# Performance work log

Hardware: AMD Instinct MI355X
Metric: run time of the kernel (lower is better)

The kernel has to match this reference:

```python
import jax, jax.numpy as jnp
import numpy as np

B, C, H, W = 8, 512, 96, 96
C8 = C // 8


def conv1x1(x, w, b):
    # x: (B,Cin,H,W), w: (Cout,Cin), b: (Cout,)
    return jnp.einsum('bchw,oc->bohw', x, w) + b[None, :, None, None]


def setup_inputs() -> dict:
    key = jax.random.key(0)
    ks = jax.random.split(key, 12)
    s = 0.05
    return {
        'x_exmplar': jax.random.normal(ks[0], (B, C, H, W), jnp.float32),
        'x_query': jax.random.normal(ks[1], (B, C, H, W), jnp.float32),
        'Wq': jax.random.normal(ks[2], (C8, C), jnp.float32) * s,
        'bq': jax.random.normal(ks[3], (C8,), jnp.float32) * s,
        'Wk': jax.random.normal(ks[4], (C8, C), jnp.float32) * s,
        'bk': jax.random.normal(ks[5], (C8,), jnp.float32) * s,
        'Wv': jax.random.normal(ks[6], (C, C), jnp.float32) * s,
        'bv': jax.random.normal(ks[7], (C,), jnp.float32) * s,
        'Wqv': jax.random.normal(ks[8], (C, C), jnp.float32) * s,
        'bqv': jax.random.normal(ks[9], (C,), jnp.float32) * s,
        'gamma1': jax.random.normal(ks[10], (1,), jnp.float32) * 0.5,
        'gamma2': jax.random.normal(ks[11], (1,), jnp.float32) * 0.5,
    }


def reference(x_exmplar, x_query, Wq, bq, Wk, bk, Wv, bv, Wqv, bqv, gamma1, gamma2):
    Bq, Cq, Hh, Ww = x_query.shape
    q = conv1x1(x_query, Wq, bq)        # (B,C8,H,W)
    k = conv1x1(x_exmplar, Wk, bk)      # (B,C8,H,W)
    v = conv1x1(x_exmplar, Wv, bv)      # (B,C,H,W)
    qv = conv1x1(x_query, Wqv, bqv)     # (B,C,H,W)

    # Criss-cross energies. energy_H masks the self position (INF diag).
    eH = jnp.einsum('bchw,bcjw->bhwj', q, k)            # (B,H,W,H)
    eye = jnp.eye(Hh, dtype=bool)                        # (H,H)
    eH = jnp.where(eye[:, None, :], -jnp.inf, eH)        # mask h==j
    eW = jnp.einsum('bchw,bchj->bhwj', q, k)             # (B,H,W,W)

    att = jax.nn.softmax(jnp.concatenate([eH, eW], axis=3), axis=3)
    att_H, att_W = att[..., :Hh], att[..., Hh:]          # (B,H,W,H),(B,H,W,W)

    out_H = jnp.einsum('bcjw,bhwj->bchw', v, att_H)
    out_W = jnp.einsum('bchj,bhwj->bchw', v, att_W)
    qout_H = jnp.einsum('bcjw,bhwj->bchw', qv, att_H)
    qout_W = jnp.einsum('bchj,bhwj->bchw', qv, att_W)

    # Diagonal (LR/RL) terms. Note: torch.diagonal of the transposed map equals
    # the diagonal itself, so energy_RL == energy_LR (faithful to original).
    qd = jnp.diagonal(q, axis1=2, axis2=3)               # (B,C8,D)
    kd = jnp.diagonal(k, axis1=2, axis2=3)
    vd = jnp.diagonal(v, axis1=2, axis2=3)               # (B,C,D)
    qvd = jnp.diagonal(qv, axis1=2, axis2=3)
    e_LR = jnp.einsum('bci,bcj->bij', kd, qd)            # (B,D,D)

    # softmax over a size-1 trailing axis (as in the original): yields ones,
    # broadcast-added over the width dim.
    out_LR = jax.nn.softmax(jnp.einsum('bcd,bdj->bcj', vd, e_LR)[..., None], axis=3)
    out_RL = jax.nn.softmax(jnp.einsum('bcd,bdj->bcj', vd, e_LR)[..., None], axis=3)
    qout_LR = jax.nn.softmax(jnp.einsum('bcd,bdj->bcj', qvd, e_LR)[..., None], axis=3)
    qout_RL = jax.nn.softmax(jnp.einsum('bcd,bdj->bcj', qvd, e_LR)[..., None], axis=3)

    examplar_att = out_H + out_W + out_LR + out_RL       # (B,C,H,W) via broadcast
    query_att = qout_H + qout_W + qout_LR + qout_RL
    return (gamma1 * examplar_att + x_exmplar, gamma2 * query_att + x_query)
```

## Files before the change

### kernel.cpp

```cpp
#include <hip/hip_runtime.h>
#include <math.h>

#define C_   512
#define C8_  64
#define HH   96
#define WW   96
#define PP   9216
#define CP   4718592
#define C8P  589824
#define ATTN 1769472

typedef __attribute__((ext_vector_type(4))) float f32x4;
typedef __attribute__((ext_vector_type(8))) __bf16 bf16x8;
typedef __attribute__((ext_vector_type(8))) unsigned short ushort8;
typedef __attribute__((ext_vector_type(4))) unsigned short ushort4v;
typedef __attribute__((ext_vector_type(2))) unsigned short ushort2v;
typedef __attribute__((ext_vector_type(2))) float float2v;

__device__ __forceinline__ float bf2f(unsigned short u) {
    union { unsigned u; float f; } x; x.u = ((unsigned)u) << 16; return x.f;
}
__device__ __forceinline__ unsigned short f2bf(float f) {
    union { float f; unsigned u; } x; x.f = f;
    unsigned r = x.u + 0x7fffu + ((x.u >> 16) & 1u);
    return (unsigned short)(r >> 16);
}
__device__ __forceinline__ void gload16(const void* g, void* l) {
    __builtin_amdgcn_global_load_lds(
        (const __attribute__((address_space(1))) unsigned int*)g,
        (__attribute__((address_space(3))) unsigned int*)l, 16, 0, 0);
}

__global__ __launch_bounds__(256) void cast_w(
    const float* __restrict__ Wv, const float* __restrict__ Wqv,
    const float* __restrict__ Wq, const float* __restrict__ Wk,
    unsigned short* __restrict__ oV, unsigned short* __restrict__ oQV,
    unsigned short* __restrict__ oQ, unsigned short* __restrict__ oK)
{
    int y = blockIdx.y;
    int n = (y < 2) ? 262144 : 32768;
    const float* s = (y == 0) ? Wv : (y == 1) ? Wqv : (y == 2) ? Wq : Wk;
    unsigned short* d = (y == 0) ? oV : (y == 1) ? oQV : (y == 2) ? oQ : oK;
    int i = (blockIdx.x * 256 + threadIdx.x) * 4;
    if (i < n) {
        float4 v = *(const float4*)(s + i);
        ushort4v o = { f2bf(v.x), f2bf(v.y), f2bf(v.z), f2bf(v.w) };
        *(ushort4v*)(d + i) = o;
    }
}

__global__ __launch_bounds__(256) void cast_transpose_cp(
    const float* __restrict__ xq, const float* __restrict__ xe,
    unsigned short* __restrict__ xTq, unsigned short* __restrict__ xTe)
{
    int zz = blockIdx.z;
    int which = zz & 1;
    size_t b = zz >> 1;
    const float* xb = (which ? xe : xq) + b * (size_t)CP;
    unsigned short* xTb = (which ? xTe : xTq) + b * (size_t)CP;
    int p0 = blockIdx.x * 64, c0 = blockIdx.y * 64;

    __shared__ unsigned short T[64][65];
    int t = threadIdx.x;
    int pp = t & 31, cg = t >> 5;
#pragma unroll
    for (int i = 0; i < 8; ++i) {
        int c = cg + 8 * i;
        float2v v = *(const float2v*)(xb + (size_t)(c0 + c) * PP + p0 + pp * 2);
        T[c][pp * 2] = f2bf(v.x);
        T[c][pp * 2 + 1] = f2bf(v.y);
    }
    __syncthreads();
    int cp = t & 31;
#pragma unroll
    for (int i = 0; i < 8; ++i) {
        int e = t + 256 * i;
        int p = e >> 5;
        ushort2v o = { T[cp * 2][p], T[cp * 2 + 1][p] };
        *(ushort2v*)(xTb + (size_t)(p0 + p) * C_ + c0 + cp * 2) = o;
    }
}

__global__ __launch_bounds__(256) void gemm_qk(
    const unsigned short* __restrict__ Wqb, const unsigned short* __restrict__ Wkb,
    const unsigned short* __restrict__ xTq, const unsigned short* __restrict__ xTe,
    const float* __restrict__ bq, const float* __restrict__ bk,
    unsigned short* __restrict__ qout, unsigned short* __restrict__ kout)
{
    int sel = blockIdx.y;
    const unsigned short* A = sel ? Wkb : Wqb;
    const float* bias = sel ? bk : bq;
    int p0 = blockIdx.x * 128;
    size_t b = blockIdx.z;
    const unsigned short* Bb = (sel ? xTe : xTq) + b * (size_t)CP;
    unsigned short* outb = (sel ? kout : qout) + b * (size_t)C8P;

    __shared__ __align__(16) unsigned short Asm[2][64 * 32];
    __shared__ __align__(16) unsigned short Bsm[2][128 * 32];

    int tid = threadIdx.x;
    int lane = tid & 63, wid = tid >> 6;
    int wr = wid >> 1, wc = wid & 1;
    int l15 = lane & 15, l4 = lane >> 4;
    f32x4 acc[2][4] = {};

#define QK_STAGE(KT, BUF)                                                              \
    {                                                                                  \
        int k0s = (KT) * 32;                                                           \
        int c = tid;                                                                   \
        gload16(A + (size_t)(c >> 2) * 512 + k0s + (c & 3) * 8, Asm[BUF] + c * 8);     \
        gload16(Bb + (size_t)(p0 + (c >> 2)) * 512 + k0s + (c & 3) * 8, Bsm[BUF] + c * 8); \
        int cb = tid + 256;                                                            \
        gload16(Bb + (size_t)(p0 + (cb >> 2)) * 512 + k0s + (cb & 3) * 8, Bsm[BUF] + cb * 8); \
    }

    QK_STAGE(0, 0);
    QK_STAGE(1, 1);

#pragma unroll
    for (int k = 0; k < 16; ++k) {
        int cur = k & 1;
        if (k < 15) asm volatile("s_waitcnt vmcnt(3)" ::: "memory");
        else        asm volatile("s_waitcnt vmcnt(0)" ::: "memory");
        __builtin_amdgcn_s_barrier();
        bf16x8 af[2], bfr[4];
#pragma unroll
        for (int m = 0; m < 2; ++m)
            af[m] = *(const bf16x8*)&Asm[cur][(wr * 32 + m * 16 + l15) * 32 + l4 * 8];
#pragma unroll
        for (int n = 0; n < 4; ++n)
            bfr[n] = *(const bf16x8*)&Bsm[cur][(wc * 64 + n * 16 + l15) * 32 + l4 * 8];
#pragma unroll
        for (int m = 0; m < 2; ++m)
#pragma unroll
            for (int n = 0; n < 4; ++n)
                acc[m][n] = __builtin_amdgcn_mfma_f32_16x16x32_bf16(af[m], bfr[n], acc[m][n], 0, 0, 0);
        asm volatile("" ::: "memory");
        __builtin_amdgcn_s_barrier();
        if (k < 14) QK_STAGE(k + 2, cur);
    }
#undef QK_STAGE

#pragma unroll
    for (int m = 0; m < 2; ++m)
#pragma unroll
        for (int n = 0; n < 4; ++n) {
            int pcol = p0 + wc * 64 + n * 16 + l15;
#pragma unroll
            for (int r = 0; r < 4; ++r) {
                int orow = wr * 32 + m * 16 + l4 * 4 + r;
                outb[(size_t)orow * PP + pcol] = f2bf(acc[m][n][r] + bias[orow]);
            }
        }
}

__global__ __launch_bounds__(256) void thw_b(
    const unsigned short* __restrict__ in, unsigned short* __restrict__ out)
{
    size_t m = blockIdx.x;
    const unsigned short* im = in + m * (size_t)PP;
    unsigned short* om = out + m * (size_t)PP;
    __shared__ unsigned short T[96][97];
    int t = threadIdx.x;
#pragma unroll
    for (int i = 0; i < 18; ++i) {
        int v = t + 256 * i;
        int r = v / 48, pp = v - r * 48;
        ushort2v u = *(const ushort2v*)(im + r * 96 + pp * 2);
        T[r][pp * 2] = u.x;
        T[r][pp * 2 + 1] = u.y;
    }
    __syncthreads();
#pragma unroll
    for (int i = 0; i < 18; ++i) {
        int v = t + 256 * i;
        int w = v / 48, hh = v - w * 48;
        ushort2v o = { T[hh * 2][w], T[hh * 2 + 1][w] };
        *(ushort2v*)(om + w * 96 + hh * 2) = o;
    }
}

__global__ __launch_bounds__(256) void scores_kernel(
    const unsigned short* __restrict__ qT, const unsigned short* __restrict__ kT,
    const unsigned short* __restrict__ q, const unsigned short* __restrict__ k,
    unsigned short* __restrict__ attb, float* __restrict__ rsum0, float* __restrict__ rsum1)
{
    int s = blockIdx.x;
    int ori = blockIdx.y;
    size_t b = blockIdx.z;
    const unsigned short* qs = (ori ? q : qT) + b * (size_t)C8P;
    const unsigned short* ks = (ori ? k : kT) + b * (size_t)C8P;
    unsigned short* ab = attb + b * (size_t)ATTN;
    float* rs = (ori ? rsum1 : rsum0) + b * (size_t)PP;

    __shared__ float Qs[64][97];
    __shared__ float Ks[64][97];
    int t = threadIdx.x;
    for (int v = t; v < 64 * 12; v += 256) {
        int c = v / 12, gg = v - c * 12;
        size_t gi = (size_t)c * PP + (size_t)s * 96 + gg * 8;
        ushort8 uq = *(const ushort8*)(qs + gi);
        ushort8 uk = *(const ushort8*)(ks + gi);
#pragma unroll
        for (int kk = 0; kk < 8; ++kk) {
            Qs[c][gg * 8 + kk] = bf2f(uq[kk]);
            Ks[c][gg * 8 + kk] = bf2f(uk[kk]);
        }
    }
    __syncthreads();
    int tx = t & 15, ty = t >> 4;
    float acc[6][6] = {};
    for (int c = 0; c < 64; ++c) {
        float qf[6], kf[6];
#pragma unroll
        for (int i = 0; i < 6; ++i) { qf[i] = Qs[c][ty + 16 * i]; kf[i] = Ks[c][tx + 16 * i]; }
#pragma unroll
        for (int i = 0; i < 6; ++i)
#pragma unroll
            for (int j = 0; j < 6; ++j) acc[i][j] = fmaf(qf[i], kf[j], acc[i][j]);
    }
#pragma unroll
    for (int i = 0; i < 6; ++i) {
        int m = ty + 16 * i;
        size_t row = ori ? ((size_t)s * 96 + m) : ((size_t)m * 96 + s);
        unsigned short* rowp = ab + row * 192 + (ori ? 96 : 0);
        float part = 0.0f;
#pragma unroll
        for (int j = 0; j < 6; ++j) {
            int jj = tx + 16 * j;
            float e = (!ori && jj == m) ? 0.0f : __expf(acc[i][j] - 20.0f);
            part += e;
            rowp[jj] = f2bf(e);
        }
#pragma unroll
        for (int off = 1; off < 16; off <<= 1) part += __shfl_xor(part, off);
        if (tx == 0) rs[row] = part;
    }
}

template<int ORI>
__global__ __launch_bounds__(512) void apply_mfma(
    const unsigned short* __restrict__ xT_e, const unsigned short* __restrict__ xT_q,
    unsigned short* __restrict__ yT_e, unsigned short* __restrict__ yT_q,
    const unsigned short* __restrict__ attb,
    const float* __restrict__ rsum0, const float* __restrict__ rsum1)
{
    int s = blockIdx.x;
    int path = blockIdx.y >> 1, ct = blockIdx.y & 1;
    int c0 = ct * 256;
    size_t b = blockIdx.z;
    const unsigned short* X = (path ? xT_q : xT_e) + b * (size_t)CP;
    unsigned short* Y = (path ? yT_q : yT_e) + b * (size_t)CP;
    const unsigned short* ab = attb + b * (size_t)ATTN;
    const float* r0 = rsum0 + b * (size_t)PP;
    const float* r1 = rsum1 + b * (size_t)PP;

    __shared__ __align__(16) unsigned short Att[96][104];
    __shared__ __align__(16) unsigned short Xs[256][104];
    __shared__ float rs_[96];

    int tid = threadIdx.x;
    for (int v = tid; v < 96 * 12; v += 512) {
        int r = v / 12, gg = v - r * 12;
        size_t base = ORI ? ((size_t)(s * 96 + r) * 192 + 96) : ((size_t)(r * 96 + s) * 192);
        *(ushort8*)&Att[r][gg * 8] = *(const ushort8*)(ab + base + gg * 8);
    }
    for (int v = tid; v < 96 * 32; v += 512) {
        int j = v >> 5, cc = v & 31;
        size_t pj = ORI ? ((size_t)s * 96 + j) : ((size_t)j * 96 + s);
        ushort8 u = *(const ushort8*)(X + pj * C_ + c0 + cc * 8);
        int js = j ^ ((cc & 3) << 3);
#pragma unroll
        for (int e = 0; e < 8; ++e) Xs[cc * 8 + e][js] = u[e];
    }
    if (ORI && tid < 96) {
        size_t p = (size_t)s * 96 + tid;
        rs_[tid] = 1.0f / (r0[p] + r1[p]);
    }
    __syncthreads();

    int lane = tid & 63, wid = tid >> 6;
    int wm = wid >> 2, wn = wid & 3;
    int l15 = lane & 15, l4 = lane >> 4;
    f32x4 acc[3][4] = {};
#pragma unroll
    for (int k = 0; k < 3; ++k) {
        bf16x8 a[3], xx[4];
#pragma unroll
        for (int mi = 0; mi < 3; ++mi)
            a[mi] = *(const bf16x8*)&Att[wm * 48 + mi * 16 + l15][k * 32 + l4 * 8];
#pragma unroll
        for (int ni = 0; ni < 4; ++ni) {
            int row = wn * 64 + ni * 16 + l15;
            int gsw = (k * 4 + l4) ^ ((row >> 3) & 3);
            xx[ni] = *(const bf16x8*)&Xs[row][gsw * 8];
        }
#pragma unroll
        for (int mi = 0; mi < 3; ++mi)
#pragma unroll
            for (int ni = 0; ni < 4; ++ni)
                acc[mi][ni] = __builtin_amdgcn_mfma_f32_16x16x32_bf16(a[mi], xx[ni], acc[mi][ni], 0, 0, 0);
    }

    unsigned short* Wf = &Xs[0][0];
    __syncthreads();
#pragma unroll
    for (int mi = 0; mi < 3; ++mi)
#pragma unroll
        for (int r = 0; r < 4; ++r) {
            int mrow = wm * 48 + mi * 16 + l4 * 4 + r;
#pragma unroll
            for (int ni = 0; ni < 4; ++ni)
                Wf[mrow * 268 + wn * 64 + ni * 16 + l15] = f2bf(acc[mi][ni][r]);
        }
    __syncthreads();
#pragma unroll
    for (int i = 0; i < 6; ++i) {
        int id = tid + 512 * i;
        int row = id >> 5, cg = id & 31;
        ushort4v w0 = *(const ushort4v*)&Wf[row * 268 + cg * 8];
        ushort4v w1 = *(const ushort4v*)&Wf[row * 268 + cg * 8 + 4];
        size_t p = ORI ? ((size_t)s * 96 + row) : ((size_t)row * 96 + s);
        unsigned short* yp = Y + p * C_ + c0 + cg * 8;
        if (ORI == 0) {
            ushort8 o = { w0[0], w0[1], w0[2], w0[3], w1[0], w1[1], w1[2], w1[3] };
            *(ushort8*)yp = o;
        } else {
            ushort8 yo = *(const ushort8*)yp;
            float rinv = rs_[row];
            ushort8 o;
#pragma unroll
            for (int e = 0; e < 4; ++e) o[e] = f2bf((bf2f(yo[e]) + bf2f(w0[e])) * rinv);
#pragma unroll
            for (int e = 0; e < 4; ++e) o[e + 4] = f2bf((bf2f(yo[e + 4]) + bf2f(w1[e])) * rinv);
            *(ushort8*)yp = o;
        }
    }
}

__global__ __launch_bounds__(512) void gemm_out(
    const unsigned short* __restrict__ Wvb, const unsigned short* __restrict__ Wqvb,
    const unsigned short* __restrict__ yT_e, const unsigned short* __restrict__ yT_q,
    const float* __restrict__ bv, const float* __restrict__ bqv,
    const float* __restrict__ xe, const float* __restrict__ xq,
    const float* __restrict__ g1, const float* __restrict__ g2,
    float* __restrict__ o0, float* __restrict__ o1)
{
    int lin = blockIdx.x + 72 * blockIdx.y;
    int nid = (lin & 7) * 72 + (lin >> 3);
    int path = nid / 288;
    int rem = nid - path * 288;
    int ptile = rem >> 2, ot = rem & 3;

    const unsigned short* A = path ? Wqvb : Wvb;
    const float* bias = path ? bqv : bv;
    int p0 = ptile * 128;
    int o0r = ot * 128;
    size_t b = blockIdx.z;
    const unsigned short* Bb = (path ? yT_q : yT_e) + b * (size_t)CP;
    const float* xb = (path ? xq : xe) + b * (size_t)CP;
    float* ob = (path ? o1 : o0) + b * (size_t)CP;
    float gam = (path ? g2 : g1)[0];

    __shared__ __align__(16) unsigned short Asm[2][128 * 64];
    __shared__ __align__(16) unsigned short Bsm[2][128 * 64];

    int tid = threadIdx.x;
    int lane = tid & 63, wid = tid >> 6;
    int wr = wid >> 2, wc = wid & 3;
    int l15 = lane & 15, l4 = lane >> 4;
    f32x4 acc[4][2] = {};
    float xv[4][2][4];

#define GO_STAGE(KT, BUF)                                                                  \
    {                                                                                      \
        int k0s = (KT) * 64;                                                               \
        _Pragma("unroll")                                                                  \
        for (int i = 0; i < 2; ++i) {                                                      \
            int ch = tid + i * 512;                                                        \
            int row = ch >> 3, slot = ch & 7;                                              \
            int gs = slot ^ (row & 7);                                                     \
            gload16(A + (size_t)(o0r + row) * 512 + k0s + gs * 8, Asm[BUF] + ch * 8);      \
            gload16(Bb + (size_t)(p0 + row) * 512 + k0s + gs * 8, Bsm[BUF] + ch * 8);      \
        }                                                                                  \
    }

    GO_STAGE(0, 0);
    GO_STAGE(1, 1);

#pragma unroll
    for (int k = 0; k < 8; ++k) {
        int cur = k & 1;
        if (k == 0)      asm volatile("s_waitcnt vmcnt(4)" ::: "memory");
        else if (k < 7)  asm volatile("s_waitcnt vmcnt(8)" ::: "memory");
        else             asm volatile("s_waitcnt vmcnt(4)" ::: "memory");
        __builtin_amdgcn_s_barrier();
#pragma unroll
        for (int ks = 0; ks < 2; ++ks) {
            bf16x8 af[4], bfr[2];
#pragma unroll
            for (int m = 0; m < 4; ++m) {
                int row = wr * 64 + m * 16 + l15;
                int sl = (ks * 4 + l4) ^ (row & 7);
                af[m] = *(const bf16x8*)&Asm[cur][row * 64 + sl * 8];
            }
#pragma unroll
            for (int n = 0; n < 2; ++n) {
                int row = wc * 32 + n * 16 + l15;
                int sl = (ks * 4 + l4) ^ (row & 7);
                bfr[n] = *(const bf16x8*)&Bsm[cur][row * 64 + sl * 8];
            }
#pragma unroll
            for (int m = 0; m < 4; ++m)
#pragma unroll
                for (int n = 0; n < 2; ++n)
                    acc[m][n] = __builtin_amdgcn_mfma_f32_16x16x32_bf16(af[m], bfr[n], acc[m][n], 0, 0, 0);
        }
        asm volatile("" ::: "memory");
        __builtin_amdgcn_s_barrier();
        {
            int xm = k >> 1, xn = k & 1;
            int pcol = p0 + wc * 32 + xn * 16 + l15;
#pragma unroll
            for (int r = 0; r < 4; ++r) {
                int orow = o0r + wr * 64 + xm * 16 + l4 * 4 + r;
                xv[xm][xn][r] = xb[(size_t)orow * PP + pcol];
            }
        }
        if (k < 6) GO_STAGE(k + 2, cur);
    }
#undef GO_STAGE
    asm volatile("s_waitcnt vmcnt(0)" ::: "memory");

#pragma unroll
    for (int m = 0; m < 4; ++m)
#pragma unroll
        for (int n = 0; n < 2; ++n) {
            int pcol = p0 + wc * 32 + n * 16 + l15;
#pragma unroll
            for (int r = 0; r < 4; ++r) {
                int orow = o0r + wr * 64 + m * 16 + l4 * 4 + r;
                size_t idx = (size_t)orow * PP + pcol;
                float val = acc[m][n][r] + bias[orow];
                ob[idx] = gam * (val + 2.0f) + xv[m][n][r];
            }
        }
}

extern "C" void kernel_launch(void* const* d_in, const int* in_sizes, int n_in,
                              void* d_out, int out_size, void* d_ws, size_t ws_size,
                              hipStream_t stream)
{
    const float* x_ex = (const float*)d_in[0];
    const float* x_q  = (const float*)d_in[1];
    const float* Wq   = (const float*)d_in[2];
    const float* bq   = (const float*)d_in[3];
    const float* Wk   = (const float*)d_in[4];
    const float* bk   = (const float*)d_in[5];
    const float* Wv   = (const float*)d_in[6];
    const float* bv   = (const float*)d_in[7];
    const float* Wqv  = (const float*)d_in[8];
    const float* bqv  = (const float*)d_in[9];
    const float* g1   = (const float*)d_in[10];
    const float* g2   = (const float*)d_in[11];
    float* out0 = (float*)d_out;
    float* out1 = out0 + (size_t)8 * CP;

    unsigned short* hp = (unsigned short*)d_ws;
    unsigned short* Wvb  = hp; hp += 262144;
    unsigned short* Wqvb = hp; hp += 262144;
    unsigned short* Wqb  = hp; hp += 32768;
    unsigned short* Wkb  = hp; hp += 32768;
    size_t head = (size_t)(hp - (unsigned short*)d_ws) * 2;

    size_t perB = 4ull * CP + (size_t)ATTN + 4ull * C8P + 4ull * PP;
    int g = 8;
    while (g > 1 && head + (size_t)g * perB * 2 > ws_size) g >>= 1;

    unsigned short* p = hp;
    unsigned short* xT_e = p; p += (size_t)g * CP;
    unsigned short* xT_q = p; p += (size_t)g * CP;
    unsigned short* yT_e = p; p += (size_t)g * CP;
    unsigned short* yT_q = p; p += (size_t)g * CP;
    unsigned short* attb = p; p += (size_t)g * ATTN;
    unsigned short* qb   = p; p += (size_t)g * C8P;
    unsigned short* kb   = p; p += (size_t)g * C8P;
    unsigned short* qTb  = p; p += (size_t)g * C8P;
    unsigned short* kTb  = p; p += (size_t)g * C8P;
    float* rsum0 = (float*)p; p += (size_t)g * PP * 2;
    float* rsum1 = (float*)p; p += (size_t)g * PP * 2;

    cast_w<<<dim3(256, 4), 256, 0, stream>>>(Wv, Wqv, Wq, Wk, Wvb, Wqvb, Wqb, Wkb);

    for (int b0 = 0; b0 < 8; b0 += g) {
        const float* xe = x_ex + (size_t)b0 * CP;
        const float* xq = x_q  + (size_t)b0 * CP;
        float* o0 = out0 + (size_t)b0 * CP;
        float* o1 = out1 + (size_t)b0 * CP;

        cast_transpose_cp<<<dim3(144, 8, 2 * g), 256, 0, stream>>>(xq, xe, xT_q, xT_e);
        gemm_qk<<<dim3(72, 2, g), 256, 0, stream>>>(Wqb, Wkb, xT_q, xT_e, bq, bk, qb, kb);
        thw_b<<<dim3(2 * g * 64), 256, 0, stream>>>(qb, qTb);
        scores_kernel<<<dim3(96, 2, g), 256, 0, stream>>>(qTb, kTb, qb, kb, attb, rsum0, rsum1);
        apply_mfma<0><<<dim3(96, 4, g), 512, 0, stream>>>(xT_e, xT_q, yT_e, yT_q, attb, rsum0, rsum1);
        apply_mfma<1><<<dim3(96, 4, g), 512, 0, stream>>>(xT_e, xT_q, yT_e, yT_q, attb, rsum0, rsum1);
        gemm_out<<<dim3(72, 8, g), 512, 0, stream>>>(Wvb, Wqvb, yT_e, yT_q, bv, bqv,
                                                     xe, xq, g1, g2, o0, o1);
    }
}
```

Measured before the change: 545.6 us.

## Defer softmax normalization to output GEMM and vectorize LDS transpose stores

Moves the softmax row-sum reciprocal scaling out of the second apply kernel into the gemm_out epilogue. This is valid because the per-pixel scale commutes with the 1x1 conv, so the apply kernel now writes an unnormalized sum. It also changes the X tile transpose into LDS so each thread loads four consecutive pixels and writes 4-wide vectors instead of scalar shared-memory stores. The risk is a small precision change, since unnormalized values are now stored in bf16 before scaling.

```diff
diff --git a/kernel.cpp b/kernel.cpp
--- a/kernel.cpp
+++ b/kernel.cpp
@@ -242,8 +242,7 @@
 __global__ __launch_bounds__(512) void apply_mfma(
     const unsigned short* __restrict__ xT_e, const unsigned short* __restrict__ xT_q,
     unsigned short* __restrict__ yT_e, unsigned short* __restrict__ yT_q,
-    const unsigned short* __restrict__ attb,
-    const float* __restrict__ rsum0, const float* __restrict__ rsum1)
+    const unsigned short* __restrict__ attb)
 {
     int s = blockIdx.x;
     int path = blockIdx.y >> 1, ct = blockIdx.y & 1;
@@ -252,12 +251,9 @@
     const unsigned short* X = (path ? xT_q : xT_e) + b * (size_t)CP;
     unsigned short* Y = (path ? yT_q : yT_e) + b * (size_t)CP;
     const unsigned short* ab = attb + b * (size_t)ATTN;
-    const float* r0 = rsum0 + b * (size_t)PP;
-    const float* r1 = rsum1 + b * (size_t)PP;
 
     __shared__ __align__(16) unsigned short Att[96][104];
     __shared__ __align__(16) unsigned short Xs[256][104];
-    __shared__ float rs_[96];
 
     int tid = threadIdx.x;
     for (int v = tid; v < 96 * 12; v += 512) {
@@ -265,17 +261,26 @@
         size_t base = ORI ? ((size_t)(s * 96 + r) * 192 + 96) : ((size_t)(r * 96 + s) * 192);
         *(ushort8*)&Att[r][gg * 8] = *(const ushort8*)(ab + base + gg * 8);
     }
-    for (int v = tid; v < 96 * 32; v += 512) {
-        int j = v >> 5, cc = v & 31;
-        size_t pj = ORI ? ((size_t)s * 96 + j) : ((size_t)j * 96 + s);
-        ushort8 u = *(const ushort8*)(X + pj * C_ + c0 + cc * 8);
-        int js = j ^ ((cc & 3) << 3);
-#pragma unroll
-        for (int e = 0; e < 8; ++e) Xs[cc * 8 + e][js] = u[e];
-    }
-    if (ORI && tid < 96) {
-        size_t p = (size_t)s * 96 + tid;
-        rs_[tid] = 1.0f / (r0[p] + r1[p]);
+#pragma unroll
+    for (int i = 0; i < 2; ++i) {
+        int id = tid + 512 * i;
+        if (id < 768) {
+            int jq = id >> 5, cc = id & 31;
+            int j = jq * 4;
+            size_t stepP = ORI ? 1 : 96;
+            size_t pj = ORI ? ((size_t)s * 96 + j) : ((size_t)j * 96 + s);
+            const unsigned short* xp = X + pj * C_ + c0 + cc * 8;
+            ushort8 u0 = *(const ushort8*)(xp);
+            ushort8 u1 = *(const ushort8*)(xp + stepP * C_);
+            ushort8 u2 = *(const ushort8*)(xp + 2 * stepP * C_);
+            ushort8 u3 = *(const ushort8*)(xp + 3 * stepP * C_);
+            int js = j ^ ((cc & 3) << 3);
+#pragma unroll
+            for (int e = 0; e < 8; ++e) {
+                ushort4v o = { u0[e], u1[e], u2[e], u3[e] };
+                *(ushort4v*)&Xs[cc * 8 + e][js] = o;
+            }
+        }
     }
     __syncthreads();
 
@@ -327,12 +332,11 @@
             *(ushort8*)yp = o;
         } else {
             ushort8 yo = *(const ushort8*)yp;
-            float rinv = rs_[row];
             ushort8 o;
 #pragma unroll
-            for (int e = 0; e < 4; ++e) o[e] = f2bf((bf2f(yo[e]) + bf2f(w0[e])) * rinv);
-#pragma unroll
-            for (int e = 0; e < 4; ++e) o[e + 4] = f2bf((bf2f(yo[e + 4]) + bf2f(w1[e])) * rinv);
+            for (int e = 0; e < 4; ++e) o[e] = f2bf(bf2f(yo[e]) + bf2f(w0[e]));
+#pragma unroll
+            for (int e = 0; e < 4; ++e) o[e + 4] = f2bf(bf2f(yo[e + 4]) + bf2f(w1[e]));
             *(ushort8*)yp = o;
         }
     }
@@ -344,6 +348,7 @@
     const float* __restrict__ bv, const float* __restrict__ bqv,
     const float* __restrict__ xe, const float* __restrict__ xq,
     const float* __restrict__ g1, const float* __restrict__ g2,
+    const float* __restrict__ rsum0, const float* __restrict__ rsum1,
     float* __restrict__ o0, float* __restrict__ o1)
 {
     int lin = blockIdx.x + 72 * blockIdx.y;
@@ -432,6 +437,14 @@
 #undef GO_STAGE
     asm volatile("s_waitcnt vmcnt(0)" ::: "memory");
 
+    float ri[2];
+#pragma unroll
+    for (int n = 0; n < 2; ++n) {
+        int pcol = p0 + wc * 32 + n * 16 + l15;
+        size_t pg = b * (size_t)PP + pcol;
+        ri[n] = 1.0f / (rsum0[pg] + rsum1[pg]);
+    }
+
 #pragma unroll
     for (int m = 0; m < 4; ++m)
 #pragma unroll
@@ -441,7 +454,7 @@
             for (int r = 0; r < 4; ++r) {
                 int orow = o0r + wr * 64 + m * 16 + l4 * 4 + r;
                 size_t idx = (size_t)orow * PP + pcol;
-                float val = acc[m][n][r] + bias[orow];
+                float val = acc[m][n][r] * ri[n] + bias[orow];
                 ob[idx] = gam * (val + 2.0f) + xv[m][n][r];
             }
         }
@@ -502,9 +515,9 @@
         gemm_qk<<<dim3(72, 2, g), 256, 0, stream>>>(Wqb, Wkb, xT_q, xT_e, bq, bk, qb, kb);
         thw_b<<<dim3(2 * g * 64), 256, 0, stream>>>(qb, qTb);
         scores_kernel<<<dim3(96, 2, g), 256, 0, stream>>>(qTb, kTb, qb, kb, attb, rsum0, rsum1);
-        apply_mfma<0><<<dim3(96, 4, g), 512, 0, stream>>>(xT_e, xT_q, yT_e, yT_q, attb, rsum0, rsum1);
-        apply_mfma<1><<<dim3(96, 4, g), 512, 0, stream>>>(xT_e, xT_q, yT_e, yT_q, attb, rsum0, rsum1);
+        apply_mfma<0><<<dim3(96, 4, g), 512, 0, stream>>>(xT_e, xT_q, yT_e, yT_q, attb);
+        apply_mfma<1><<<dim3(96, 4, g), 512, 0, stream>>>(xT_e, xT_q, yT_e, yT_q, attb);
         gemm_out<<<dim3(72, 8, g), 512, 0, stream>>>(Wvb, Wqvb, yT_e, yT_q, bv, bqv,
-                                                     xe, xq, g1, g2, o0, o1);
-    }
-}
+                                                     xe, xq, g1, g2, rsum0, rsum1, o0, o1);
+    }
+}
```

Measured after the change: 522.3 us. 1.04x faster.
